# Kernel tuning notes

Measured on AMD Instinct MI355X. Metric: run time of the kernel, lower is better.

Reference implementation:

```python
import jax, jax.numpy as jnp
import numpy as np

DIM = 1024
NUM_HEADS = 16
HEAD_DIM = DIM // NUM_HEADS
SCALE = HEAD_DIM ** -0.5


def setup_inputs() -> dict:
    key = jax.random.key(0)
    k_x, k_qkv, k_pw, k_pb = jax.random.split(key, 4)
    B, S = 2, 2048
    x = jax.random.normal(k_x, (B, S, DIM), dtype=jnp.float32)
    # nn.Linear(dim, 3*dim, bias=False): weight [3*dim, dim]
    w_qkv = jax.random.normal(k_qkv, (3 * DIM, DIM), dtype=jnp.float32) * (DIM ** -0.5)
    # nn.Linear(dim, dim): weight [dim, dim], bias [dim]
    w_proj = jax.random.normal(k_pw, (DIM, DIM), dtype=jnp.float32) * (DIM ** -0.5)
    b_proj = jax.random.normal(k_pb, (DIM,), dtype=jnp.float32) * 0.01
    return {"x": x, "w_qkv": w_qkv, "w_proj": w_proj, "b_proj": b_proj}


def reference(x, w_qkv, w_proj, b_proj):
    B, S, D = x.shape
    qkv = jnp.einsum("bsd,ed->bse", x, w_qkv)  # [B,S,3D]
    q, k, v = jnp.split(qkv, 3, axis=-1)
    def heads(t):  # [B,S,D] -> [B,H,S,hd]
        return t.reshape(B, S, NUM_HEADS, HEAD_DIM).transpose(0, 2, 1, 3)
    q, k, v = heads(q), heads(k), heads(v)
    attn = jnp.einsum("bhqd,bhkd->bhqk", q, k) * SCALE  # [B,H,S,S]
    attn = jax.nn.softmax(attn, axis=-1)
    out = jnp.einsum("bhqk,bhkd->bhqd", attn, v)  # [B,H,S,hd]
    out = out.transpose(0, 2, 1, 3).reshape(B, S, D)
    return jnp.einsum("bsd,ed->bse", out, w_proj) + b_proj
```

## Files before the change

kernel.cpp:

```cpp
#include <hip/hip_runtime.h>
#include <stdint.h>

typedef __bf16 bf16;
typedef __bf16 bf16x8 __attribute__((ext_vector_type(8)));
typedef float f32x4 __attribute__((ext_vector_type(4)));
typedef float f32x16 __attribute__((ext_vector_type(16)));

typedef __attribute__((address_space(1))) void gvoid_t;
typedef __attribute__((address_space(3))) void lvoid_t;

__device__ __forceinline__ void gload16(const void* src, void* lds) {
    __builtin_amdgcn_global_load_lds((gvoid_t*)src, (lvoid_t*)lds, 16, 0, 0);
}

__device__ __forceinline__ float fexp2(float x) {
    float r;
    asm("v_exp_f32 %0, %1" : "=v"(r) : "v"(x));
    return r;
}

__global__ __launch_bounds__(256) void cvt3_kernel(const float* __restrict__ x,
                                                   const float* __restrict__ wqkv,
                                                   const float* __restrict__ wproj,
                                                   bf16* __restrict__ xb,
                                                   bf16* __restrict__ wqkvb,
                                                   bf16* __restrict__ wprojb) {
    int idx = blockIdx.x * 256 + threadIdx.x;
    int stride = gridDim.x * 256;
    for (int i = idx; i < 1048576; i += stride) {
        const float* in;
        bf16* out;
        int j;
        if (i < 524288) { in = x; out = xb; j = i; }
        else if (i < 917504) { in = wqkv; out = wqkvb; j = i - 524288; }
        else { in = wproj; out = wprojb; j = i - 917504; }
        const float4* p = (const float4*)in;
        float4 a = p[(long)j * 2], b = p[(long)j * 2 + 1];
        bf16x8 o;
        o[0] = (bf16)a.x; o[1] = (bf16)a.y; o[2] = (bf16)a.z; o[3] = (bf16)a.w;
        o[4] = (bf16)b.x; o[5] = (bf16)b.y; o[6] = (bf16)b.z; o[7] = (bf16)b.w;
        ((bf16x8*)out)[j] = o;
    }
}

template <bool F32OUT, int BN>
__global__ __launch_bounds__(256) void gemm_bt(const bf16* __restrict__ A,
                                               const bf16* __restrict__ W,
                                               const float* __restrict__ bias,
                                               void* __restrict__ Cout,
                                               const int M, const int N, const int K) {
    constexpr int NT = BN / 32;
    constexpr int BELEMS = BN * 32;
    __shared__ __align__(16) bf16 Alds[3 * 4096];
    __shared__ __align__(16) bf16 Blds[3 * BELEMS];
    const int t = threadIdx.x;
    const int wid = t >> 6, lane = t & 63;
    const int g = lane >> 4, c = lane & 15;
    const int wm = wid >> 1, wn = wid & 1;
    const long bm = (long)blockIdx.y * 128, bn = (long)blockIdx.x * BN;

    f32x4 acc[4][NT] = {};

    const int arow = t >> 2;
    const int acol = (t & 3) * 8;
    const bf16* Asrc = A + (bm + arow) * (long)K + acol;
    const bf16* Bsrc = W + (bn + arow) * (long)K + acol;
    const int dstb = wid * 512;

#define GSTAGE(BI)                                                       \
    {                                                                    \
        bf16* ad = Alds + (BI) * 4096 + dstb;                            \
        bf16* bd = Blds + (BI) * BELEMS + dstb;                          \
        gload16(Asrc, ad);                                               \
        gload16(Asrc + (long)64 * K, ad + 2048);                         \
        gload16(Bsrc, bd);                                               \
        if constexpr (BN == 128) gload16(Bsrc + (long)64 * K, bd + 2048);\
        Asrc += 32;                                                      \
        Bsrc += 32;                                                      \
    }

    auto computeg = [&](int bi) __attribute__((always_inline)) {
        const bf16* Ab = Alds + bi * 4096;
        const bf16* Bb = Blds + bi * BELEMS;
        bf16x8 af[4], bfr[NT];
#pragma unroll
        for (int mt = 0; mt < 4; ++mt)
            af[mt] = *(const bf16x8*)(Ab + (wm * 64 + mt * 16 + c) * 32 + g * 8);
#pragma unroll
        for (int nt = 0; nt < NT; ++nt)
            bfr[nt] = *(const bf16x8*)(Bb + (wn * (BN / 2) + nt * 16 + c) * 32 + g * 8);
#pragma unroll
        for (int mt = 0; mt < 4; ++mt)
#pragma unroll
            for (int nt = 0; nt < NT; ++nt)
                acc[mt][nt] = __builtin_amdgcn_mfma_f32_16x16x32_bf16(af[mt], bfr[nt],
                                                                      acc[mt][nt], 0, 0, 0);
    };

#define GWAITN                                                              \
    if constexpr (BN == 128) { asm volatile("s_waitcnt vmcnt(4)" ::: "memory"); } \
    else { asm volatile("s_waitcnt vmcnt(3)" ::: "memory"); }

#define GSTEP(CUR, NXT)            \
    GWAITN;                        \
    __builtin_amdgcn_s_barrier();  \
    GSTAGE(NXT);                   \
    computeg(CUR);

    GSTAGE(0);
    GSTAGE(1);
    for (int t3 = 0; t3 < 10; ++t3) {
        GSTEP(0, 2)
        GSTEP(1, 0)
        GSTEP(2, 1)
    }
    GWAITN;
    __builtin_amdgcn_s_barrier();
    computeg(0);
    asm volatile("s_waitcnt vmcnt(0)" ::: "memory");
    __builtin_amdgcn_s_barrier();
    computeg(1);
#undef GSTEP
#undef GWAITN
#undef GSTAGE

#pragma unroll
    for (int mt = 0; mt < 4; ++mt) {
#pragma unroll
        for (int nt = 0; nt < NT; ++nt) {
#pragma unroll
            for (int i = 0; i < 4; ++i) {
                const long row = bm + wm * 64 + mt * 16 + g * 4 + i;
                const long col = bn + wn * (BN / 2) + nt * 16 + c;
                if constexpr (F32OUT) {
                    ((float*)Cout)[row * N + col] = acc[mt][nt][i] + bias[col];
                } else {
                    ((bf16*)Cout)[row * N + col] = (bf16)acc[mt][nt][i];
                }
            }
        }
    }
}

__global__ __launch_bounds__(256) void flash_kernel(const bf16* __restrict__ qk,
                                                    const bf16* __restrict__ Vt,
                                                    bf16* __restrict__ attno) {
    __shared__ __align__(16) bf16 KV[24576];
    __shared__ float LP[128];

    const int t = threadIdx.x;
    const int wid = t >> 6, lane = t & 63;
    const int l31 = lane & 31, hl = lane >> 5;

    const int i0 = blockIdx.x;
    const int xcd = i0 & 7, slot = i0 >> 3;
    const int bh = xcd * 4 + (slot >> 4);
    const int qb = slot & 15;
    const int b = bh >> 4, h = bh & 15;
    const int rowbase = b * 2048;
    const int q0w = qb * 128 + wid * 32;

    bf16x8 qf[4];
    {
        const bf16* qrow = qk + (long)(rowbase + q0w + l31) * 2048 + h * 64 + hl * 8;
        const float qs = 0.18033688f;
#pragma unroll
        for (int ks = 0; ks < 4; ++ks) {
            bf16x8 a = *(const bf16x8*)(qrow + ks * 16);
#pragma unroll
            for (int e = 0; e < 8; ++e) qf[ks][e] = (bf16)((float)a[e] * qs);
        }
    }

    const int srow = t >> 3, sq = t & 7;
    const int swcol = (sq ^ (srow & 7)) * 8;
    const bf16* ksn = qk + (long)(rowbase + srow) * 2048 + 1024 + h * 64 + swcol;
    const bf16* vsn = Vt + (long)(h * 64 + srow) * 4096 + b * 2048 + swcol;
    const int kchunk = wid * 512;

    int rdoff[4];
#pragma unroll
    for (int ks = 0; ks < 4; ++ks)
        rdoff[ks] = l31 * 64 + (((ks * 2 + hl) ^ (l31 & 7)) * 8);

    float lpA = 0.f, lpB = 0.f, lpC = 0.f, lpD = 0.f;
    f32x16 oacc0 = {}, oacc1 = {};

#define STAGE(BI)                                                        \
    {                                                                    \
        bf16* kd = KV + (BI) * 4096 + kchunk;                            \
        bf16* vd = KV + 12288 + (BI) * 4096 + kchunk;                    \
        gload16(ksn, kd);                                                \
        gload16(ksn + 65536, kd + 2048);                                 \
        gload16(vsn, vd);                                                \
        gload16(vsn + 131072, vd + 2048);                                \
        ksn += 131072;                                                   \
        vsn += 64;                                                       \
    }

    auto compute = [&](int bi) __attribute__((always_inline)) {
        const bf16* Kb = KV + bi * 4096;
        const bf16* Vb = KV + 12288 + bi * 4096;
        f32x16 s0 = {}, s1 = {};
        __builtin_amdgcn_s_setprio(1);
#pragma unroll
        for (int ks = 0; ks < 4; ++ks) {
            bf16x8 kf0 = *(const bf16x8*)(Kb + rdoff[ks]);
            bf16x8 kf1 = *(const bf16x8*)(Kb + 2048 + rdoff[ks]);
            s0 = __builtin_amdgcn_mfma_f32_32x32x16_bf16(kf0, qf[ks], s0, 0, 0, 0);
            s1 = __builtin_amdgcn_mfma_f32_32x32x16_bf16(kf1, qf[ks], s1, 0, 0, 0);
        }
        __builtin_amdgcn_s_setprio(0);
        float p0[16], p1[16];
#pragma unroll
        for (int r = 0; r < 16; ++r) p0[r] = fexp2(s0[r]);
#pragma unroll
        for (int r = 0; r < 16; ++r) p1[r] = fexp2(s1[r]);
#pragma unroll
        for (int r = 0; r < 4; ++r) {
            lpA += p0[r * 4 + 0] + p1[r * 4 + 0];
            lpB += p0[r * 4 + 1] + p1[r * 4 + 1];
            lpC += p0[r * 4 + 2] + p1[r * 4 + 2];
            lpD += p0[r * 4 + 3] + p1[r * 4 + 3];
        }
        __builtin_amdgcn_s_setprio(1);
#pragma unroll
        for (int ks = 0; ks < 4; ++ks) {
            const float* pp = (ks < 2) ? p0 : p1;
            const int s = (ks & 1) * 8;
            unsigned wA, wB, wC, wD;
            asm("v_cvt_pk_bf16_f32 %0, %1, %2" : "=v"(wA) : "v"(pp[s + 0]), "v"(pp[s + 1]));
            asm("v_cvt_pk_bf16_f32 %0, %1, %2" : "=v"(wB) : "v"(pp[s + 4]), "v"(pp[s + 5]));
            asm("v_cvt_pk_bf16_f32 %0, %1, %2" : "=v"(wC) : "v"(pp[s + 2]), "v"(pp[s + 3]));
            asm("v_cvt_pk_bf16_f32 %0, %1, %2" : "=v"(wD) : "v"(pp[s + 6]), "v"(pp[s + 7]));
            asm("v_permlane32_swap_b32 %0, %1" : "+v"(wA), "+v"(wB));
            asm("v_permlane32_swap_b32 %0, %1" : "+v"(wC), "+v"(wD));
            union { unsigned w[4]; bf16x8 v; } pu;
            pu.w[0] = wA; pu.w[1] = wC; pu.w[2] = wB; pu.w[3] = wD;
            bf16x8 vf0 = *(const bf16x8*)(Vb + rdoff[ks]);
            bf16x8 vf1 = *(const bf16x8*)(Vb + 2048 + rdoff[ks]);
            oacc0 = __builtin_amdgcn_mfma_f32_32x32x16_bf16(pu.v, vf0, oacc0, 0, 0, 0);
            oacc1 = __builtin_amdgcn_mfma_f32_32x32x16_bf16(pu.v, vf1, oacc1, 0, 0, 0);
        }
        __builtin_amdgcn_s_setprio(0);
    };

    STAGE(0);
    STAGE(1);

#define FSTEP(CUR, NXT)                                    \
    asm volatile("s_waitcnt vmcnt(4)" ::: "memory");       \
    __builtin_amdgcn_s_barrier();                          \
    STAGE(NXT);                                            \
    compute(CUR);

    for (int t3 = 0; t3 < 10; ++t3) {
        FSTEP(0, 2)
        FSTEP(1, 0)
        FSTEP(2, 1)
    }
    asm volatile("s_waitcnt vmcnt(4)" ::: "memory");
    __builtin_amdgcn_s_barrier();
    compute(0);
    asm volatile("s_waitcnt vmcnt(0)" ::: "memory");
    __builtin_amdgcn_s_barrier();
    compute(1);
#undef FSTEP
#undef STAGE

    float lpart = (lpA + lpB) + (lpC + lpD);
    lpart += __shfl_xor(lpart, 32);
    if (lane < 32) LP[wid * 32 + l31] = lpart;
    float inv[16];
#pragma unroll
    for (int r = 0; r < 16; ++r) {
        const int qrow = (r & 3) + 8 * (r >> 2) + 4 * hl;
        inv[r] = 1.0f / LP[wid * 32 + qrow];
    }

#pragma unroll
    for (int r = 0; r < 16; ++r) {
        const int qrow = (r & 3) + 8 * (r >> 2) + 4 * hl;
        const long rbase = (long)(rowbase + q0w + qrow) * 1024 + h * 64 + l31;
        attno[rbase] = (bf16)(oacc0[r] * inv[r]);
        attno[rbase + 32] = (bf16)(oacc1[r] * inv[r]);
    }
}

extern "C" void kernel_launch(void* const* d_in, const int* in_sizes, int n_in,
                              void* d_out, int out_size, void* d_ws, size_t ws_size,
                              hipStream_t stream) {
    const float* x = (const float*)d_in[0];
    const float* wqkv = (const float*)d_in[1];
    const float* wproj = (const float*)d_in[2];
    const float* bproj = (const float*)d_in[3];

    char* ws = (char*)d_ws;
    bf16* xb     = (bf16*)(ws);
    bf16* wqkvb  = (bf16*)(ws + 8388608);
    bf16* wprojb = (bf16*)(ws + 14680064);
    bf16* qk     = (bf16*)(ws + 16777216);
    bf16* Vt     = (bf16*)(ws + 33554432);
    bf16* attno  = (bf16*)(ws + 41943040);
    if (ws_size < 50331648) return;

    cvt3_kernel<<<2048, 256, 0, stream>>>(x, wqkv, wproj, xb, wqkvb, wprojb);

    gemm_bt<false, 128><<<dim3(16, 32), 256, 0, stream>>>(xb, wqkvb, nullptr, qk,
                                                          4096, 2048, 1024);

    gemm_bt<false, 64><<<dim3(64, 8), 256, 0, stream>>>(wqkvb + 2048 * 1024, xb, nullptr, Vt,
                                                        1024, 4096, 1024);

    flash_kernel<<<512, 256, 0, stream>>>(qk, Vt, attno);

    gemm_bt<true, 64><<<dim3(16, 32), 256, 0, stream>>>(attno, wprojb, bproj, d_out,
                                                        4096, 1024, 1024);
}
```

Baseline: 124.3 us.

## Give each flash wave 64 query rows with two warps, widen GEMM tiles

The flash kernel now runs 2 waves per block, each handling 64 query rows split into two 32-row subtiles that share every K/V fragment read from LDS. Staging issues twice as many loads per thread so the same tile is filled, and the wait counts are raised to match. The V-projection and output-projection GEMMs switch to the 128-wide tile variant with fewer blocks. This trades more registers per wave and fewer waves per block for less LDS traffic per MFMA. It also risks lower occupancy and fewer blocks on the GEMMs.

```diff
diff --git a/kernel.cpp b/kernel.cpp
--- a/kernel.cpp
+++ b/kernel.cpp
@@ -142,7 +142,7 @@
     }
 }
 
-__global__ __launch_bounds__(256) void flash_kernel(const bf16* __restrict__ qk,
+__global__ __launch_bounds__(128) void flash_kernel(const bf16* __restrict__ qk,
                                                     const bf16* __restrict__ Vt,
                                                     bf16* __restrict__ attno) {
     __shared__ __align__(16) bf16 KV[24576];
@@ -158,24 +158,29 @@
     const int qb = slot & 15;
     const int b = bh >> 4, h = bh & 15;
     const int rowbase = b * 2048;
-    const int q0w = qb * 128 + wid * 32;
-
-    bf16x8 qf[4];
+    const int q0w = qb * 128 + wid * 64;
+
+    bf16x8 qfa[4], qfb[4];
     {
-        const bf16* qrow = qk + (long)(rowbase + q0w + l31) * 2048 + h * 64 + hl * 8;
+        const bf16* qra = qk + (long)(rowbase + q0w + l31) * 2048 + h * 64 + hl * 8;
+        const bf16* qrb = qra + 32 * 2048;
         const float qs = 0.18033688f;
 #pragma unroll
         for (int ks = 0; ks < 4; ++ks) {
-            bf16x8 a = *(const bf16x8*)(qrow + ks * 16);
-#pragma unroll
-            for (int e = 0; e < 8; ++e) qf[ks][e] = (bf16)((float)a[e] * qs);
-        }
-    }
-
-    const int srow = t >> 3, sq = t & 7;
-    const int swcol = (sq ^ (srow & 7)) * 8;
-    const bf16* ksn = qk + (long)(rowbase + srow) * 2048 + 1024 + h * 64 + swcol;
-    const bf16* vsn = Vt + (long)(h * 64 + srow) * 4096 + b * 2048 + swcol;
+            bf16x8 a = *(const bf16x8*)(qra + ks * 16);
+            bf16x8 d = *(const bf16x8*)(qrb + ks * 16);
+#pragma unroll
+            for (int e = 0; e < 8; ++e) {
+                qfa[ks][e] = (bf16)((float)a[e] * qs);
+                qfb[ks][e] = (bf16)((float)d[e] * qs);
+            }
+        }
+    }
+
+    const int srow0 = wid * 8 + ((lane >> 3) & 7);
+    const int swcol = ((lane & 7) ^ (srow0 & 7)) * 8;
+    const bf16* ksn = qk + (long)(rowbase + srow0) * 2048 + 1024 + h * 64 + swcol;
+    const bf16* vsn = Vt + (long)(h * 64 + srow0) * 4096 + b * 2048 + swcol;
     const int kchunk = wid * 512;
 
     int rdoff[4];
@@ -183,17 +188,21 @@
     for (int ks = 0; ks < 4; ++ks)
         rdoff[ks] = l31 * 64 + (((ks * 2 + hl) ^ (l31 & 7)) * 8);
 
-    float lpA = 0.f, lpB = 0.f, lpC = 0.f, lpD = 0.f;
-    f32x16 oacc0 = {}, oacc1 = {};
+    float lpA0 = 0.f, lpB0 = 0.f, lpA1 = 0.f, lpB1 = 0.f;
+    f32x16 oacc00 = {}, oacc10 = {}, oacc01 = {}, oacc11 = {};
 
 #define STAGE(BI)                                                        \
     {                                                                    \
         bf16* kd = KV + (BI) * 4096 + kchunk;                            \
         bf16* vd = KV + 12288 + (BI) * 4096 + kchunk;                    \
         gload16(ksn, kd);                                                \
+        gload16(ksn + 32768, kd + 1024);                                 \
         gload16(ksn + 65536, kd + 2048);                                 \
+        gload16(ksn + 98304, kd + 3072);                                 \
         gload16(vsn, vd);                                                \
+        gload16(vsn + 65536, vd + 1024);                                 \
         gload16(vsn + 131072, vd + 2048);                                \
+        gload16(vsn + 196608, vd + 3072);                                \
         ksn += 131072;                                                   \
         vsn += 64;                                                       \
     }
@@ -201,46 +210,68 @@
     auto compute = [&](int bi) __attribute__((always_inline)) {
         const bf16* Kb = KV + bi * 4096;
         const bf16* Vb = KV + 12288 + bi * 4096;
-        f32x16 s0 = {}, s1 = {};
+        f32x16 s00 = {}, s10 = {}, s01 = {}, s11 = {};
         __builtin_amdgcn_s_setprio(1);
 #pragma unroll
         for (int ks = 0; ks < 4; ++ks) {
             bf16x8 kf0 = *(const bf16x8*)(Kb + rdoff[ks]);
             bf16x8 kf1 = *(const bf16x8*)(Kb + 2048 + rdoff[ks]);
-            s0 = __builtin_amdgcn_mfma_f32_32x32x16_bf16(kf0, qf[ks], s0, 0, 0, 0);
-            s1 = __builtin_amdgcn_mfma_f32_32x32x16_bf16(kf1, qf[ks], s1, 0, 0, 0);
+            s00 = __builtin_amdgcn_mfma_f32_32x32x16_bf16(kf0, qfa[ks], s00, 0, 0, 0);
+            s10 = __builtin_amdgcn_mfma_f32_32x32x16_bf16(kf1, qfa[ks], s10, 0, 0, 0);
+            s01 = __builtin_amdgcn_mfma_f32_32x32x16_bf16(kf0, qfb[ks], s01, 0, 0, 0);
+            s11 = __builtin_amdgcn_mfma_f32_32x32x16_bf16(kf1, qfb[ks], s11, 0, 0, 0);
         }
         __builtin_amdgcn_s_setprio(0);
-        float p0[16], p1[16];
-#pragma unroll
-        for (int r = 0; r < 16; ++r) p0[r] = fexp2(s0[r]);
-#pragma unroll
-        for (int r = 0; r < 16; ++r) p1[r] = fexp2(s1[r]);
-#pragma unroll
-        for (int r = 0; r < 4; ++r) {
-            lpA += p0[r * 4 + 0] + p1[r * 4 + 0];
-            lpB += p0[r * 4 + 1] + p1[r * 4 + 1];
-            lpC += p0[r * 4 + 2] + p1[r * 4 + 2];
-            lpD += p0[r * 4 + 3] + p1[r * 4 + 3];
+        float p00[16], p10[16], p01[16], p11[16];
+#pragma unroll
+        for (int r = 0; r < 16; ++r) p00[r] = fexp2(s00[r]);
+#pragma unroll
+        for (int r = 0; r < 16; ++r) p10[r] = fexp2(s10[r]);
+#pragma unroll
+        for (int r = 0; r < 16; ++r) p01[r] = fexp2(s01[r]);
+#pragma unroll
+        for (int r = 0; r < 16; ++r) p11[r] = fexp2(s11[r]);
+#pragma unroll
+        for (int r = 0; r < 8; ++r) {
+            lpA0 += p00[r] + p10[r];
+            lpB0 += p00[r + 8] + p10[r + 8];
+            lpA1 += p01[r] + p11[r];
+            lpB1 += p01[r + 8] + p11[r + 8];
         }
         __builtin_amdgcn_s_setprio(1);
 #pragma unroll
         for (int ks = 0; ks < 4; ++ks) {
-            const float* pp = (ks < 2) ? p0 : p1;
-            const int s = (ks & 1) * 8;
-            unsigned wA, wB, wC, wD;
-            asm("v_cvt_pk_bf16_f32 %0, %1, %2" : "=v"(wA) : "v"(pp[s + 0]), "v"(pp[s + 1]));
-            asm("v_cvt_pk_bf16_f32 %0, %1, %2" : "=v"(wB) : "v"(pp[s + 4]), "v"(pp[s + 5]));
-            asm("v_cvt_pk_bf16_f32 %0, %1, %2" : "=v"(wC) : "v"(pp[s + 2]), "v"(pp[s + 3]));
-            asm("v_cvt_pk_bf16_f32 %0, %1, %2" : "=v"(wD) : "v"(pp[s + 6]), "v"(pp[s + 7]));
-            asm("v_permlane32_swap_b32 %0, %1" : "+v"(wA), "+v"(wB));
-            asm("v_permlane32_swap_b32 %0, %1" : "+v"(wC), "+v"(wD));
-            union { unsigned w[4]; bf16x8 v; } pu;
-            pu.w[0] = wA; pu.w[1] = wC; pu.w[2] = wB; pu.w[3] = wD;
             bf16x8 vf0 = *(const bf16x8*)(Vb + rdoff[ks]);
             bf16x8 vf1 = *(const bf16x8*)(Vb + 2048 + rdoff[ks]);
-            oacc0 = __builtin_amdgcn_mfma_f32_32x32x16_bf16(pu.v, vf0, oacc0, 0, 0, 0);
-            oacc1 = __builtin_amdgcn_mfma_f32_32x32x16_bf16(pu.v, vf1, oacc1, 0, 0, 0);
+            const int s = (ks & 1) * 8;
+            {
+                const float* pp = (ks < 2) ? p00 : p10;
+                unsigned wA, wB, wC, wD;
+                asm("v_cvt_pk_bf16_f32 %0, %1, %2" : "=v"(wA) : "v"(pp[s + 0]), "v"(pp[s + 1]));
+                asm("v_cvt_pk_bf16_f32 %0, %1, %2" : "=v"(wB) : "v"(pp[s + 4]), "v"(pp[s + 5]));
+                asm("v_cvt_pk_bf16_f32 %0, %1, %2" : "=v"(wC) : "v"(pp[s + 2]), "v"(pp[s + 3]));
+                asm("v_cvt_pk_bf16_f32 %0, %1, %2" : "=v"(wD) : "v"(pp[s + 6]), "v"(pp[s + 7]));
+                asm("v_permlane32_swap_b32 %0, %1" : "+v"(wA), "+v"(wB));
+                asm("v_permlane32_swap_b32 %0, %1" : "+v"(wC), "+v"(wD));
+                union { unsigned w[4]; bf16x8 v; } pu;
+                pu.w[0] = wA; pu.w[1] = wC; pu.w[2] = wB; pu.w[3] = wD;
+                oacc00 = __builtin_amdgcn_mfma_f32_32x32x16_bf16(pu.v, vf0, oacc00, 0, 0, 0);
+                oacc10 = __builtin_amdgcn_mfma_f32_32x32x16_bf16(pu.v, vf1, oacc10, 0, 0, 0);
+            }
+            {
+                const float* pp = (ks < 2) ? p01 : p11;
+                unsigned wA, wB, wC, wD;
+                asm("v_cvt_pk_bf16_f32 %0, %1, %2" : "=v"(wA) : "v"(pp[s + 0]), "v"(pp[s + 1]));
+                asm("v_cvt_pk_bf16_f32 %0, %1, %2" : "=v"(wB) : "v"(pp[s + 4]), "v"(pp[s + 5]));
+                asm("v_cvt_pk_bf16_f32 %0, %1, %2" : "=v"(wC) : "v"(pp[s + 2]), "v"(pp[s + 3]));
+                asm("v_cvt_pk_bf16_f32 %0, %1, %2" : "=v"(wD) : "v"(pp[s + 6]), "v"(pp[s + 7]));
+                asm("v_permlane32_swap_b32 %0, %1" : "+v"(wA), "+v"(wB));
+                asm("v_permlane32_swap_b32 %0, %1" : "+v"(wC), "+v"(wD));
+                union { unsigned w[4]; bf16x8 v; } pu;
+                pu.w[0] = wA; pu.w[1] = wC; pu.w[2] = wB; pu.w[3] = wD;
+                oacc01 = __builtin_amdgcn_mfma_f32_32x32x16_bf16(pu.v, vf0, oacc01, 0, 0, 0);
+                oacc11 = __builtin_amdgcn_mfma_f32_32x32x16_bf16(pu.v, vf1, oacc11, 0, 0, 0);
+            }
         }
         __builtin_amdgcn_s_setprio(0);
     };
@@ -249,7 +280,7 @@
     STAGE(1);
 
 #define FSTEP(CUR, NXT)                                    \
-    asm volatile("s_waitcnt vmcnt(4)" ::: "memory");       \
+    asm volatile("s_waitcnt vmcnt(8)" ::: "memory");       \
     __builtin_amdgcn_s_barrier();                          \
     STAGE(NXT);                                            \
     compute(CUR);
@@ -259,7 +290,7 @@
         FSTEP(1, 0)
         FSTEP(2, 1)
     }
-    asm volatile("s_waitcnt vmcnt(4)" ::: "memory");
+    asm volatile("s_waitcnt vmcnt(8)" ::: "memory");
     __builtin_amdgcn_s_barrier();
     compute(0);
     asm volatile("s_waitcnt vmcnt(0)" ::: "memory");
@@ -268,22 +299,27 @@
 #undef FSTEP
 #undef STAGE
 
-    float lpart = (lpA + lpB) + (lpC + lpD);
-    lpart += __shfl_xor(lpart, 32);
-    if (lane < 32) LP[wid * 32 + l31] = lpart;
-    float inv[16];
+    float lp0 = lpA0 + lpB0;
+    float lp1 = lpA1 + lpB1;
+    lp0 += __shfl_xor(lp0, 32);
+    lp1 += __shfl_xor(lp1, 32);
+    if (lane < 32) {
+        LP[wid * 64 + l31] = lp0;
+        LP[wid * 64 + 32 + l31] = lp1;
+    }
+    __builtin_amdgcn_s_barrier();
+
 #pragma unroll
     for (int r = 0; r < 16; ++r) {
         const int qrow = (r & 3) + 8 * (r >> 2) + 4 * hl;
-        inv[r] = 1.0f / LP[wid * 32 + qrow];
-    }
-
-#pragma unroll
-    for (int r = 0; r < 16; ++r) {
-        const int qrow = (r & 3) + 8 * (r >> 2) + 4 * hl;
-        const long rbase = (long)(rowbase + q0w + qrow) * 1024 + h * 64 + l31;
-        attno[rbase] = (bf16)(oacc0[r] * inv[r]);
-        attno[rbase + 32] = (bf16)(oacc1[r] * inv[r]);
+        const float i0v = 1.0f / LP[wid * 64 + qrow];
+        const float i1v = 1.0f / LP[wid * 64 + 32 + qrow];
+        const long rb0 = (long)(rowbase + q0w + qrow) * 1024 + h * 64 + l31;
+        const long rb1 = (long)(rowbase + q0w + 32 + qrow) * 1024 + h * 64 + l31;
+        attno[rb0] = (bf16)(oacc00[r] * i0v);
+        attno[rb0 + 32] = (bf16)(oacc10[r] * i0v);
+        attno[rb1] = (bf16)(oacc01[r] * i1v);
+        attno[rb1 + 32] = (bf16)(oacc11[r] * i1v);
     }
 }
 
@@ -309,11 +345,11 @@
     gemm_bt<false, 128><<<dim3(16, 32), 256, 0, stream>>>(xb, wqkvb, nullptr, qk,
                                                           4096, 2048, 1024);
 
-    gemm_bt<false, 64><<<dim3(64, 8), 256, 0, stream>>>(wqkvb + 2048 * 1024, xb, nullptr, Vt,
-                                                        1024, 4096, 1024);
-
-    flash_kernel<<<512, 256, 0, stream>>>(qk, Vt, attno);
-
-    gemm_bt<true, 64><<<dim3(16, 32), 256, 0, stream>>>(attno, wprojb, bproj, d_out,
+    gemm_bt<false, 128><<<dim3(32, 8), 256, 0, stream>>>(wqkvb + 2048 * 1024, xb, nullptr, Vt,
+                                                         1024, 4096, 1024);
+
+    flash_kernel<<<512, 128, 0, stream>>>(qk, Vt, attno);
+
+    gemm_bt<true, 128><<<dim3(8, 32), 256, 0, stream>>>(attno, wprojb, bproj, d_out,
                                                         4096, 1024, 1024);
 }
```

New measurement: 133.7 us. 7.6% more time.
